# Optimization experiments

Hardware: AMD Instinct MI355X
Metric: run time of the kernel (lower is better)

The kernel has to match this reference:

```python
import jax, jax.numpy as jnp
import numpy as np

HEADS = 8
DIM_HEAD = 64
BN_EPS = 1e-5

def setup_inputs() -> dict:
    key = jax.random.key(0)
    ks = jax.random.split(key, 6)
    B, N, D = 8, 1024, 512
    inner = HEADS * DIM_HEAD  # 512
    return {
        "x": jax.random.normal(ks[0], (B, N, D), dtype=jnp.float32),
        "w_qkv": jax.random.normal(ks[1], (D, 3 * inner), dtype=jnp.float32) * (D ** -0.5),
        "conv_w": jax.random.normal(ks[2], (HEADS, HEADS), dtype=jnp.float32) * (HEADS ** -0.5),
        "conv_b": jax.random.normal(ks[3], (HEADS,), dtype=jnp.float32) * 0.02,
        "bn_gamma": jnp.ones((HEADS,), dtype=jnp.float32),
        "bn_beta": jnp.zeros((HEADS,), dtype=jnp.float32),
        "w_out": jax.random.normal(ks[4], (inner, D), dtype=jnp.float32) * (inner ** -0.5),
        "b_out": jnp.zeros((D,), dtype=jnp.float32),
    }

def reference(x, w_qkv, conv_w, conv_b, bn_gamma, bn_beta, w_out, b_out):
    B, N, D = x.shape
    H, dh = HEADS, DIM_HEAD
    scale = dh ** -0.5
    qkv = x @ w_qkv  # [B, N, 3*H*dh]
    q, k, v = jnp.split(qkv, 3, axis=-1)
    # b n (h d) -> b h n d
    q = q.reshape(B, N, H, dh).transpose(0, 2, 1, 3)
    k = k.reshape(B, N, H, dh).transpose(0, 2, 1, 3)
    v = v.reshape(B, N, H, dh).transpose(0, 2, 1, 3)
    attn = jnp.einsum('bhnd,bhmd->bhnm', q, k) * scale
    attn = jax.nn.softmax(attn, axis=-1)
    # 1x1 conv across heads (channels = heads)
    attn = jnp.einsum('gh,bhnm->bgnm', conv_w, attn) + conv_b[None, :, None, None]
    # BatchNorm2d in training mode: batch stats over (B, N, N) per head, biased variance
    mean = attn.mean(axis=(0, 2, 3), keepdims=True)
    var = attn.var(axis=(0, 2, 3), keepdims=True)
    attn = (attn - mean) * jax.lax.rsqrt(var + BN_EPS)
    attn = attn * bn_gamma[None, :, None, None] + bn_beta[None, :, None, None]
    # reatten_scale = 1.0 (transform_scale=False)
    out = jnp.einsum('bhnm,bhmd->bhnd', attn, v)
    out = out.transpose(0, 2, 1, 3).reshape(B, N, H * dh)  # b h n d -> b n (h d)
    return out @ w_out + b_out
```

## Files before the change

### kernel.cpp

```cpp
#include <hip/hip_runtime.h>
#include <math.h>


#define Bz 8
#define Nn 1024
#define Dd 512
#define Hh 8
#define DH 64
#define INNER 512
#define QW 1536
#define SCALE 0.125f
#define BN_EPS 1e-5f

typedef _Float16 __f16;
typedef __f16 f16x8 __attribute__((ext_vector_type(8)));
typedef float f32x4 __attribute__((ext_vector_type(4)));

#define MFMA16(a, b, c) __builtin_amdgcn_mfma_f32_16x16x32_f16((a), (b), (c), 0, 0, 0)

__device__ __forceinline__ unsigned short f2h(float f) {
  union { __f16 h; unsigned short s; } v;
  v.h = (__f16)f;
  return v.s;
}
__device__ __forceinline__ float h2f(unsigned short s) {
  union { unsigned short s; __f16 h; } v;
  v.s = s;
  return (float)v.h;
}

#define WB_XB 0u
#define WB_QKV 8388608u
#define WB_O1 0u
#define WB_VT 33554432u
#define WB_SG 41943040u
#define WB_O1BF WB_SG
#define WB_WQT 176160768u
#define WB_WOT 177733632u
#define WB_RSUM 178257920u
#define WB_VSUM 178520064u
#define WB_STATS 178536448u
#define WB_AC 178536512u

__global__ __launch_bounds__(256) void k_xbf(const float* __restrict__ X,
                                             unsigned short* __restrict__ XB) {
  const size_t i = ((size_t)blockIdx.x * 256 + threadIdx.x) * 8;
  float4 f0 = *(const float4*)(X + i);
  float4 f1 = *(const float4*)(X + i + 4);
  unsigned short o[8] = {f2h(f0.x), f2h(f0.y), f2h(f0.z), f2h(f0.w),
                         f2h(f1.x), f2h(f1.y), f2h(f1.z), f2h(f1.w)};
  *(uint4*)(XB + i) = *(uint4*)o;
}

__global__ __launch_bounds__(256) void k_transpose(const float* __restrict__ src,
                                                   unsigned short* __restrict__ dst,
                                                   int R, int C) {
  __shared__ float tile[32][33];
  const int tc = blockIdx.x * 32, tr = blockIdx.y * 32;
  const int lx = threadIdx.x & 31, ly = threadIdx.x >> 5;
#pragma unroll
  for (int i = 0; i < 32; i += 8)
    tile[ly + i][lx] = src[(size_t)(tr + ly + i) * C + tc + lx];
  __syncthreads();
#pragma unroll
  for (int i = 0; i < 32; i += 8)
    dst[(size_t)(tc + ly + i) * R + tr + lx] = f2h(tile[lx][ly + i]);
}

__global__ __launch_bounds__(256) void k_qkv(const unsigned short* __restrict__ XB,
                                             const unsigned short* __restrict__ WQT,
                                             unsigned short* __restrict__ qkv,
                                             unsigned short* __restrict__ vT) {
  extern __shared__ char smem[];
  unsigned short(*sA)[40] = (unsigned short(*)[40])smem;
  unsigned short(*sB)[40] = (unsigned short(*)[40])(smem + 128 * 40 * 2);
  unsigned short* sEp = (unsigned short*)smem;
  const int t = threadIdx.x;
  const int col0 = blockIdx.x * 128;
  const int row0 = blockIdx.y * 128;
  const bool isqk = (col0 < 2 * INNER);
  const int l = t & 63, w = t >> 6;
  const int wm = (w & 1) * 64, wn = (w >> 1) * 64;
  const int lm = l & 15, lq = l >> 4;
  const int srow = t >> 1, skc = (t & 1) * 16;
  f32x4 acc[4][4] = {};
  for (int k0 = 0; k0 < Dd; k0 += 32) {
    {
      const unsigned short* src = XB + (size_t)(row0 + srow) * Dd + k0 + skc;
      *(uint4*)&sA[srow][skc] = *(const uint4*)src;
      *(uint4*)&sA[srow][skc + 8] = *(const uint4*)(src + 8);
    }
    {
      const unsigned short* srcB = WQT + (size_t)(col0 + srow) * Dd + k0 + skc;
      *(uint4*)&sB[srow][skc] = *(const uint4*)srcB;
      *(uint4*)&sB[srow][skc + 8] = *(const uint4*)(srcB + 8);
    }
    __syncthreads();
    f16x8 af[4], bfr[4];
#pragma unroll
    for (int i = 0; i < 4; i++) af[i] = *(const f16x8*)&sA[wm + 16 * i + lm][lq * 8];
#pragma unroll
    for (int j = 0; j < 4; j++) bfr[j] = *(const f16x8*)&sB[wn + 16 * j + lm][lq * 8];
    if (isqk) {
#pragma unroll
      for (int i = 0; i < 4; i++)
#pragma unroll
        for (int j = 0; j < 4; j++) acc[i][j] = MFMA16(bfr[i], af[j], acc[i][j]);
    } else {
#pragma unroll
      for (int i = 0; i < 4; i++)
#pragma unroll
        for (int j = 0; j < 4; j++) acc[i][j] = MFMA16(af[i], bfr[j], acc[i][j]);
    }
    __syncthreads();
  }
  if (isqk) {
#pragma unroll
    for (int jc = 0; jc < 4; jc++)
#pragma unroll
      for (int ir = 0; ir < 4; ir++) {
        unsigned short us[4];
#pragma unroll
        for (int r = 0; r < 4; r++) us[r] = f2h(acc[jc][ir][r]);
        *(uint2*)&sEp[(wm + 16 * ir + lm) * 136 + wn + 16 * jc + 4 * lq] = *(uint2*)us;
      }
    __syncthreads();
    const int row = t >> 1, half = t & 1;
    const unsigned short* src = &sEp[row * 136 + half * 64];
    unsigned short* dst = qkv + (size_t)(row0 + row) * QW + col0 + half * 64;
#pragma unroll
    for (int c = 0; c < 8; c++) *(uint4*)(dst + c * 8) = *(const uint4*)(src + c * 8);
  } else {
#pragma unroll
    for (int ir = 0; ir < 4; ir++)
#pragma unroll
      for (int jc = 0; jc < 4; jc++) {
        unsigned short us[4];
#pragma unroll
        for (int r = 0; r < 4; r++) us[r] = f2h(acc[ir][jc][r]);
        *(uint2*)&sEp[(wn + 16 * jc + lm) * 136 + wm + 16 * ir + 4 * lq] = *(uint2*)us;
      }
    __syncthreads();
    const int row = t >> 1, half = t & 1;
    const int gd = col0 - 2 * INNER + row;
    const int bq = row0 >> 10, mseq0 = row0 & 1023;
    const unsigned short* src = &sEp[row * 136 + half * 64];
    unsigned short* dst =
        vT + (((size_t)(bq * Hh + (gd >> 6)) * DH + (gd & 63)) << 10) + mseq0 + half * 64;
#pragma unroll
    for (int c = 0; c < 8; c++) *(uint4*)(dst + c * 8) = *(const uint4*)(src + c * 8);
  }
}

__global__ __launch_bounds__(256) void k_vsum(const unsigned short* __restrict__ vT,
                                              float* __restrict__ vsum) {
  const int bg = blockIdx.x;
  const int d = threadIdx.x >> 2, qq = threadIdx.x & 3;
  __shared__ float red[64][4];
  const unsigned short* p = vT + ((size_t)bg * DH + d) * Nn + qq * 256;
  float s = 0.f;
  for (int m = 0; m < 256; m += 4) {
    uint2 rr = *(const uint2*)(p + m);
    s += h2f((unsigned short)(rr.x & 0xffff)) + h2f((unsigned short)(rr.x >> 16)) +
         h2f((unsigned short)(rr.y & 0xffff)) + h2f((unsigned short)(rr.y >> 16));
  }
  red[d][qq] = s;
  __syncthreads();
  if (threadIdx.x < 64)
    vsum[(size_t)bg * DH + threadIdx.x] =
        red[threadIdx.x][0] + red[threadIdx.x][1] + red[threadIdx.x][2] + red[threadIdx.x][3];
}

__global__ __launch_bounds__(512, 2) void k_sgen(const unsigned short* __restrict__ qkv,
                                                 unsigned short* __restrict__ Sg,
                                                 float* __restrict__ rsum) {
  __shared__ unsigned short sK[8 * 32 * 72];
  __shared__ unsigned short sT[32 * 264];
  const int b = blockIdx.x;
  const int n0 = blockIdx.y * 32;
  const int mh = blockIdx.z;
  const int t = threadIdx.x;
  const int w = t >> 6, l = t & 63;
  const int lm = l & 15, lq = l >> 4;
  f16x8 qf[2][2];
#pragma unroll
  for (int i = 0; i < 2; i++) {
    const unsigned short* qp =
        qkv + (size_t)(b * Nn + n0 + 16 * i + lm) * QW + w * DH + lq * 8;
    qf[i][0] = *(const f16x8*)qp;
    qf[i][1] = *(const f16x8*)(qp + 32);
  }
  float psum[2] = {0.f, 0.f};
  for (int it = 0; it < 16; it++) {
    const int m0 = mh * 512 + it * 32;
    {
#pragma unroll
      for (int s = 0; s < 4; s++) {
        const int c = t + s * 512;
        const int hh = c >> 8, mm = (c >> 3) & 31, qq = c & 7;
        *(uint4*)&sK[(hh * 32 + mm) * 72 + qq * 8] = *(const uint4*)(
            qkv + (size_t)(b * Nn + m0 + mm) * QW + INNER + hh * DH + qq * 8);
      }
    }
    __syncthreads();
    f32x4 lac[2][2] = {};
#pragma unroll
    for (int jm = 0; jm < 2; jm++) {
      f16x8 ka0 = *(const f16x8*)&sK[(w * 32 + 16 * jm + lm) * 72 + lq * 8];
      f16x8 ka1 = *(const f16x8*)&sK[(w * 32 + 16 * jm + lm) * 72 + 32 + lq * 8];
#pragma unroll
      for (int i = 0; i < 2; i++) {
        lac[i][jm] = MFMA16(ka0, qf[i][0], lac[i][jm]);
        lac[i][jm] = MFMA16(ka1, qf[i][1], lac[i][jm]);
      }
    }
#pragma unroll
    for (int i = 0; i < 2; i++)
#pragma unroll
      for (int jm = 0; jm < 2; jm++)
#pragma unroll
        for (int r = 0; r < 4; r++) {
          float e = __expf(lac[i][jm][r] * SCALE);
          psum[i] += e;
          sT[(16 * i + lm) * 264 + (16 * jm + 4 * lq + r) * 8 + w] = f2h(e);
        }
    __syncthreads();
    {
      const int row = t >> 4, ck = t & 15;
      unsigned short* dst =
          Sg + (((size_t)(b * Nn + n0 + row) << 10) + m0) * 8 + ck * 16;
      const unsigned short* src = &sT[row * 264 + ck * 16];
      *(uint4*)dst = *(const uint4*)src;
      *(uint4*)(dst + 8) = *(const uint4*)(src + 8);
    }
  }
#pragma unroll
  for (int i = 0; i < 2; i++) {
    psum[i] += __shfl_xor(psum[i], 16);
    psum[i] += __shfl_xor(psum[i], 32);
  }
  if (lq == 0) {
    atomicAdd(&rsum[(size_t)(b * Hh + w) * Nn + n0 + lm], psum[0]);
    atomicAdd(&rsum[(size_t)(b * Hh + w) * Nn + n0 + 16 + lm], psum[1]);
  }
}

__global__ __launch_bounds__(512, 2) void k_mixsv(const unsigned short* __restrict__ Sg,
                                                  const unsigned short* __restrict__ vT,
                                                  const float* __restrict__ rsum,
                                                  const float* __restrict__ conv_w,
                                                  float* __restrict__ O1,
                                                  float* __restrict__ stats) {
  __shared__ unsigned short sU[8][16][68];
  __shared__ float sRed[8][16];
  const int b = blockIdx.x;
  const int n0 = blockIdx.y * 16;
  const int t = threadIdx.x;
  const int w = t >> 6, l = t & 63;
  const int lm = l & 15, lq = l >> 4;
  const int mxn = t >> 5, mxm = (t & 31) * 2;
  float cw[64];
#pragma unroll
  for (int i = 0; i < 64; i++) cw[i] = conv_w[i];
  float rv[8];
#pragma unroll
  for (int h = 0; h < 8; h++) rv[h] = 1.0f / rsum[(size_t)(b * Hh + h) * Nn + n0 + mxn];
  const unsigned short* sNp = Sg + ((size_t)(b * Nn + n0 + mxn) << 13);
  f32x4 oacc[4] = {};
  float su[8] = {}, su2[8] = {};
  uint4 c0, c1;
  {
    const unsigned short* p = sNp + (mxm << 3);
    c0 = *(const uint4*)p;
    c1 = *(const uint4*)(p + 8);
  }
  for (int it = 0; it < 16; it++) {
    uint4 nx0, nx1;
    if (it < 15) {
      const unsigned short* p = sNp + ((size_t)((it + 1) * 64 + mxm) << 3);
      nx0 = *(const uint4*)p;
      nx1 = *(const uint4*)(p + 8);
    }
    {
      const unsigned* pe = (const unsigned*)&c0;
      const unsigned* po = (const unsigned*)&c1;
      float sx[8], sy[8];
#pragma unroll
      for (int hp = 0; hp < 4; hp++) {
        sx[2 * hp] = h2f((unsigned short)(pe[hp] & 0xffff)) * rv[2 * hp];
        sx[2 * hp + 1] = h2f((unsigned short)(pe[hp] >> 16)) * rv[2 * hp + 1];
        sy[2 * hp] = h2f((unsigned short)(po[hp] & 0xffff)) * rv[2 * hp];
        sy[2 * hp + 1] = h2f((unsigned short)(po[hp] >> 16)) * rv[2 * hp + 1];
      }
#pragma unroll
      for (int g = 0; g < 8; g++) {
        float u0 = 0.f, u1 = 0.f;
#pragma unroll
        for (int h = 0; h < 8; h++) {
          u0 += cw[g * 8 + h] * sx[h];
          u1 += cw[g * 8 + h] * sy[h];
        }
        su[g] += u0 + u1;
        su2[g] += u0 * u0 + u1 * u1;
        *(unsigned*)&sU[g][mxn][mxm] = (unsigned)f2h(u0) | ((unsigned)f2h(u1) << 16);
      }
    }
    __syncthreads();
    {
      f16x8 uf0 = *(const f16x8*)&sU[w][lm][lq * 8];
      f16x8 uf1 = *(const f16x8*)&sU[w][lm][32 + lq * 8];
#pragma unroll
      for (int j = 0; j < 4; j++) {
        const unsigned short* vp =
            vT + (((size_t)(b * Hh + w) * DH + 16 * j + lm) << 10) + it * 64 + lq * 8;
        f16x8 v0 = *(const f16x8*)vp;
        f16x8 v1 = *(const f16x8*)(vp + 32);
        oacc[j] = MFMA16(uf0, v0, oacc[j]);
        oacc[j] = MFMA16(uf1, v1, oacc[j]);
      }
    }
    __syncthreads();
    if (it < 15) {
      c0 = nx0;
      c1 = nx1;
    }
  }
#pragma unroll
  for (int j = 0; j < 4; j++)
#pragma unroll
    for (int r = 0; r < 4; r++)
      O1[((size_t)(b * Hh + w) * Nn + n0 + lq * 4 + r) * DH + 16 * j + lm] = oacc[j][r];
#pragma unroll
  for (int g = 0; g < 8; g++) {
    float a = su[g], q = su2[g];
    for (int off = 32; off; off >>= 1) {
      a += __shfl_down(a, off);
      q += __shfl_down(q, off);
    }
    if (l == 0) {
      sRed[w][g] = a;
      sRed[w][8 + g] = q;
    }
  }
  __syncthreads();
  if (t < 16) {
    float s = 0.f;
#pragma unroll
    for (int ww = 0; ww < 8; ww++) s += sRed[ww][t];
    atomicAdd(&stats[t], s);
  }
}

__global__ void k_alpha(const float* __restrict__ stats, const float* __restrict__ bn_gamma,
                        const float* __restrict__ bn_beta, float* __restrict__ ac) {
  const int g = threadIdx.x;
  if (g < 8) {
    const float cnt = (float)Bz * (float)Nn * (float)Nn;
    float Eu = stats[g] / cnt;
    float Eu2 = stats[8 + g] / cnt;
    float inv = rsqrtf(Eu2 - Eu * Eu + BN_EPS);
    float alpha = bn_gamma[g] * inv;
    ac[g] = alpha;
    ac[8 + g] = bn_beta[g] - Eu * alpha;
  }
}

__global__ __launch_bounds__(256) void k_o1aff(const float* __restrict__ O1,
                                               const float* __restrict__ vsum,
                                               const float* __restrict__ ac,
                                               unsigned short* __restrict__ O1BF) {
  const size_t i4 = ((size_t)blockIdx.x * 256 + threadIdx.x) * 4;
  const int bg = (int)(i4 >> 16);
  const int g = bg & 7;
  const int d = (int)(i4 & 63);
  float4 a = *(const float4*)(O1 + i4);
  float4 v = *(const float4*)(vsum + (size_t)bg * DH + d);
  const float al = ac[g], cc = ac[8 + g];
  unsigned short o[4] = {f2h(al * a.x + cc * v.x), f2h(al * a.y + cc * v.y),
                         f2h(al * a.z + cc * v.z), f2h(al * a.w + cc * v.w)};
  *(uint2*)(O1BF + i4) = *(uint2*)o;
}

__global__ __launch_bounds__(256) void k_out(const unsigned short* __restrict__ O1BF,
                                             const unsigned short* __restrict__ WOT,
                                             const float* __restrict__ bout,
                                             float* __restrict__ out) {
  __shared__ unsigned short sA[128][40];
  __shared__ unsigned short sB[128][40];
  const int t = threadIdx.x;
  const int col0 = blockIdx.x * 128, row0 = blockIdx.y * 128;
  const int l = t & 63, w = t >> 6;
  const int wm = (w & 1) * 64, wn = (w >> 1) * 64;
  const int lm = l & 15, lq = l >> 4;
  const int srow = t >> 1, skc = (t & 1) * 16;
  const int b = row0 >> 10;
  const int nn = (row0 + srow) & 1023;
  f32x4 acc[4][4] = {};
  for (int k0 = 0; k0 < INNER; k0 += 32) {
    {
      const int k = k0 + skc;
      const int g = k >> 6, dd = k & 63;
      const unsigned short* src = O1BF + ((size_t)(b * Hh + g) * Nn + nn) * DH + dd;
      *(uint4*)&sA[srow][skc] = *(const uint4*)src;
      *(uint4*)&sA[srow][skc + 8] = *(const uint4*)(src + 8);
    }
    {
      const unsigned short* srcB = WOT + (size_t)(col0 + srow) * INNER + k0 + skc;
      *(uint4*)&sB[srow][skc] = *(const uint4*)srcB;
      *(uint4*)&sB[srow][skc + 8] = *(const uint4*)(srcB + 8);
    }
    __syncthreads();
    f16x8 af[4], bfr[4];
#pragma unroll
    for (int i = 0; i < 4; i++) af[i] = *(const f16x8*)&sA[wm + 16 * i + lm][lq * 8];
#pragma unroll
    for (int j = 0; j < 4; j++) bfr[j] = *(const f16x8*)&sB[wn + 16 * j + lm][lq * 8];
#pragma unroll
    for (int i = 0; i < 4; i++)
#pragma unroll
      for (int j = 0; j < 4; j++) acc[i][j] = MFMA16(af[i], bfr[j], acc[i][j]);
    __syncthreads();
  }
#pragma unroll
  for (int j = 0; j < 4; j++) {
    const int col = col0 + wn + 16 * j + lm;
    const float bo = bout[col];
#pragma unroll
    for (int i = 0; i < 4; i++) {
      const int rbase = row0 + wm + 16 * i + lq * 4;
#pragma unroll
      for (int r = 0; r < 4; r++) out[(size_t)(rbase + r) * Dd + col] = acc[i][j][r] + bo;
    }
  }
}

extern "C" void kernel_launch(void* const* d_in, const int* in_sizes, int n_in,
                              void* d_out, int out_size, void* d_ws, size_t ws_size,
                              hipStream_t stream) {
  const float* x = (const float*)d_in[0];
  const float* w_qkv = (const float*)d_in[1];
  const float* conv_w = (const float*)d_in[2];
  const float* bn_gamma = (const float*)d_in[4];
  const float* bn_beta = (const float*)d_in[5];
  const float* w_out = (const float*)d_in[6];
  const float* b_out = (const float*)d_in[7];
  char* ws = (char*)d_ws;
  unsigned short* XB = (unsigned short*)(ws + WB_XB);
  unsigned short* QKV = (unsigned short*)(ws + WB_QKV);
  unsigned short* VT = (unsigned short*)(ws + WB_VT);
  unsigned short* SG = (unsigned short*)(ws + WB_SG);
  unsigned short* WQT = (unsigned short*)(ws + WB_WQT);
  unsigned short* WOT = (unsigned short*)(ws + WB_WOT);
  float* O1 = (float*)(ws + WB_O1);
  unsigned short* O1BF = (unsigned short*)(ws + WB_O1BF);
  float* RSUM = (float*)(ws + WB_RSUM);
  float* VSUM = (float*)(ws + WB_VSUM);
  float* STATS = (float*)(ws + WB_STATS);
  float* AC = (float*)(ws + WB_AC);

  hipMemsetAsync(STATS, 0, 64, stream);
  hipMemsetAsync(RSUM, 0, 262144, stream);
  k_xbf<<<2048, 256, 0, stream>>>(x, XB);
  k_transpose<<<dim3(48, 16), 256, 0, stream>>>(w_qkv, WQT, 512, 1536);
  k_transpose<<<dim3(16, 16), 256, 0, stream>>>(w_out, WOT, 512, 512);
  k_qkv<<<dim3(12, 64), 256, 34816, stream>>>(XB, WQT, QKV, VT);
  k_vsum<<<64, 256, 0, stream>>>(VT, VSUM);
  k_sgen<<<dim3(8, 32, 2), 512, 0, stream>>>(QKV, SG, RSUM);
  k_mixsv<<<dim3(8, 64), 512, 0, stream>>>(SG, VT, RSUM, conv_w, O1, STATS);
  k_alpha<<<1, 64, 0, stream>>>(STATS, bn_gamma, bn_beta, AC);
  k_o1aff<<<4096, 256, 0, stream>>>(O1, VSUM, AC, O1BF);
  k_out<<<dim3(4, 64), 256, 0, stream>>>(O1BF, WOT, b_out, (float*)d_out);
}
```

Measured before the change: 271.7 us.

## Chunk batch through sgen/mixsv and split mixsv over key halves

The score-generation and mix/SV stages now process the batch in two chunks of four, so the intermediate exp-score buffer is half as large and more likely to stay in the last-level cache between the producer and consumer kernels. mixsv also gains a grid dimension that splits the key range into two halves, writing separate partial outputs that the affine kernel sums. It double-buffers the shared U tile so one barrier per iteration can be dropped. The cost is extra kernel launches, an extra fp32 partial output buffer to read, and less parallelism per launch.

After: 303.1 us. 1.12x slower.

```diff
diff --git a/kernel.cpp b/kernel.cpp
--- a/kernel.cpp
+++ b/kernel.cpp
@@ -31,16 +31,17 @@
 
 #define WB_XB 0u
 #define WB_QKV 8388608u
-#define WB_O1 0u
 #define WB_VT 33554432u
 #define WB_SG 41943040u
-#define WB_O1BF WB_SG
-#define WB_WQT 176160768u
-#define WB_WOT 177733632u
-#define WB_RSUM 178257920u
-#define WB_VSUM 178520064u
-#define WB_STATS 178536448u
-#define WB_AC 178536512u
+#define WB_O1A 109051904u
+#define WB_O1B 125829120u
+#define WB_O1BF 142606336u
+#define WB_WQT 150994944u
+#define WB_WOT 152567808u
+#define WB_RSUM 153092096u
+#define WB_VSUM 153354240u
+#define WB_STATS 153370624u
+#define WB_AC 153370688u
 
 __global__ __launch_bounds__(256) void k_xbf(const float* __restrict__ X,
                                              unsigned short* __restrict__ XB) {
@@ -173,12 +174,12 @@
 
 __global__ __launch_bounds__(512, 2) void k_sgen(const unsigned short* __restrict__ qkv,
                                                  unsigned short* __restrict__ Sg,
-                                                 float* __restrict__ rsum) {
+                                                 float* __restrict__ rsum, int b0) {
   __shared__ unsigned short sK[8 * 32 * 72];
   __shared__ unsigned short sT[32 * 264];
-  const int b = blockIdx.x;
+  const int bl = blockIdx.x, b = b0 + bl;
   const int n0 = blockIdx.y * 32;
-  const int mh = blockIdx.z;
+  const int mq = blockIdx.z;
   const int t = threadIdx.x;
   const int w = t >> 6, l = t & 63;
   const int lm = l & 15, lq = l >> 4;
@@ -191,8 +192,8 @@
     qf[i][1] = *(const f16x8*)(qp + 32);
   }
   float psum[2] = {0.f, 0.f};
-  for (int it = 0; it < 16; it++) {
-    const int m0 = mh * 512 + it * 32;
+  for (int it = 0; it < 8; it++) {
+    const int m0 = mq * 256 + it * 32;
     {
 #pragma unroll
       for (int s = 0; s < 4; s++) {
@@ -228,7 +229,7 @@
     {
       const int row = t >> 4, ck = t & 15;
       unsigned short* dst =
-          Sg + (((size_t)(b * Nn + n0 + row) << 10) + m0) * 8 + ck * 16;
+          Sg + (((size_t)(bl * Nn + n0 + row) << 10) + m0) * 8 + ck * 16;
       const unsigned short* src = &sT[row * 264 + ck * 16];
       *(uint4*)dst = *(const uint4*)src;
       *(uint4*)(dst + 8) = *(const uint4*)(src + 8);
@@ -249,12 +250,15 @@
                                                   const unsigned short* __restrict__ vT,
                                                   const float* __restrict__ rsum,
                                                   const float* __restrict__ conv_w,
-                                                  float* __restrict__ O1,
-                                                  float* __restrict__ stats) {
-  __shared__ unsigned short sU[8][16][68];
+                                                  float* __restrict__ O1A,
+                                                  float* __restrict__ O1B,
+                                                  float* __restrict__ stats, int b0) {
+  __shared__ unsigned short sU[2][8][16][68];
   __shared__ float sRed[8][16];
-  const int b = blockIdx.x;
+  const int bl = blockIdx.x, b = b0 + bl;
   const int n0 = blockIdx.y * 16;
+  const int mbase = blockIdx.z * 512;
+  float* __restrict__ O1 = blockIdx.z ? O1B : O1A;
   const int t = threadIdx.x;
   const int w = t >> 6, l = t & 63;
   const int lm = l & 15, lq = l >> 4;
@@ -265,19 +269,20 @@
   float rv[8];
 #pragma unroll
   for (int h = 0; h < 8; h++) rv[h] = 1.0f / rsum[(size_t)(b * Hh + h) * Nn + n0 + mxn];
-  const unsigned short* sNp = Sg + ((size_t)(b * Nn + n0 + mxn) << 13);
+  const unsigned short* sNp = Sg + ((size_t)(bl * Nn + n0 + mxn) << 13);
   f32x4 oacc[4] = {};
   float su[8] = {}, su2[8] = {};
   uint4 c0, c1;
   {
-    const unsigned short* p = sNp + (mxm << 3);
+    const unsigned short* p = sNp + ((size_t)(mbase + mxm) << 3);
     c0 = *(const uint4*)p;
     c1 = *(const uint4*)(p + 8);
   }
-  for (int it = 0; it < 16; it++) {
+  for (int it = 0; it < 8; it++) {
+    const int cur = it & 1;
     uint4 nx0, nx1;
-    if (it < 15) {
-      const unsigned short* p = sNp + ((size_t)((it + 1) * 64 + mxm) << 3);
+    if (it < 7) {
+      const unsigned short* p = sNp + ((size_t)(mbase + (it + 1) * 64 + mxm) << 3);
       nx0 = *(const uint4*)p;
       nx1 = *(const uint4*)(p + 8);
     }
@@ -302,25 +307,24 @@
         }
         su[g] += u0 + u1;
         su2[g] += u0 * u0 + u1 * u1;
-        *(unsigned*)&sU[g][mxn][mxm] = (unsigned)f2h(u0) | ((unsigned)f2h(u1) << 16);
-      }
-    }
-    __syncthreads();
-    {
-      f16x8 uf0 = *(const f16x8*)&sU[w][lm][lq * 8];
-      f16x8 uf1 = *(const f16x8*)&sU[w][lm][32 + lq * 8];
+        *(unsigned*)&sU[cur][g][mxn][mxm] = (unsigned)f2h(u0) | ((unsigned)f2h(u1) << 16);
+      }
+    }
+    __syncthreads();
+    {
+      f16x8 uf0 = *(const f16x8*)&sU[cur][w][lm][lq * 8];
+      f16x8 uf1 = *(const f16x8*)&sU[cur][w][lm][32 + lq * 8];
 #pragma unroll
       for (int j = 0; j < 4; j++) {
         const unsigned short* vp =
-            vT + (((size_t)(b * Hh + w) * DH + 16 * j + lm) << 10) + it * 64 + lq * 8;
+            vT + (((size_t)(b * Hh + w) * DH + 16 * j + lm) << 10) + mbase + it * 64 + lq * 8;
         f16x8 v0 = *(const f16x8*)vp;
         f16x8 v1 = *(const f16x8*)(vp + 32);
         oacc[j] = MFMA16(uf0, v0, oacc[j]);
         oacc[j] = MFMA16(uf1, v1, oacc[j]);
       }
     }
-    __syncthreads();
-    if (it < 15) {
+    if (it < 7) {
       c0 = nx0;
       c1 = nx1;
     }
@@ -365,7 +369,8 @@
   }
 }
 
-__global__ __launch_bounds__(256) void k_o1aff(const float* __restrict__ O1,
+__global__ __launch_bounds__(256) void k_o1aff(const float* __restrict__ O1A,
+                                               const float* __restrict__ O1B,
                                                const float* __restrict__ vsum,
                                                const float* __restrict__ ac,
                                                unsigned short* __restrict__ O1BF) {
@@ -373,11 +378,12 @@
   const int bg = (int)(i4 >> 16);
   const int g = bg & 7;
   const int d = (int)(i4 & 63);
-  float4 a = *(const float4*)(O1 + i4);
+  float4 a = *(const float4*)(O1A + i4);
+  float4 bb = *(const float4*)(O1B + i4);
   float4 v = *(const float4*)(vsum + (size_t)bg * DH + d);
   const float al = ac[g], cc = ac[8 + g];
-  unsigned short o[4] = {f2h(al * a.x + cc * v.x), f2h(al * a.y + cc * v.y),
-                         f2h(al * a.z + cc * v.z), f2h(al * a.w + cc * v.w)};
+  unsigned short o[4] = {f2h(al * (a.x + bb.x) + cc * v.x), f2h(al * (a.y + bb.y) + cc * v.y),
+                         f2h(al * (a.z + bb.z) + cc * v.z), f2h(al * (a.w + bb.w) + cc * v.w)};
   *(uint2*)(O1BF + i4) = *(uint2*)o;
 }
 
@@ -451,7 +457,8 @@
   unsigned short* SG = (unsigned short*)(ws + WB_SG);
   unsigned short* WQT = (unsigned short*)(ws + WB_WQT);
   unsigned short* WOT = (unsigned short*)(ws + WB_WOT);
-  float* O1 = (float*)(ws + WB_O1);
+  float* O1Ap = (float*)(ws + WB_O1A);
+  float* O1Bp = (float*)(ws + WB_O1B);
   unsigned short* O1BF = (unsigned short*)(ws + WB_O1BF);
   float* RSUM = (float*)(ws + WB_RSUM);
   float* VSUM = (float*)(ws + WB_VSUM);
@@ -465,9 +472,12 @@
   k_transpose<<<dim3(16, 16), 256, 0, stream>>>(w_out, WOT, 512, 512);
   k_qkv<<<dim3(12, 64), 256, 34816, stream>>>(XB, WQT, QKV, VT);
   k_vsum<<<64, 256, 0, stream>>>(VT, VSUM);
-  k_sgen<<<dim3(8, 32, 2), 512, 0, stream>>>(QKV, SG, RSUM);
-  k_mixsv<<<dim3(8, 64), 512, 0, stream>>>(SG, VT, RSUM, conv_w, O1, STATS);
+  for (int c = 0; c < 2; c++) {
+    k_sgen<<<dim3(4, 32, 4), 512, 0, stream>>>(QKV, SG, RSUM, c * 4);
+    k_mixsv<<<dim3(4, 64, 2), 512, 0, stream>>>(SG, VT, RSUM, conv_w, O1Ap, O1Bp,
+                                                STATS, c * 4);
+  }
   k_alpha<<<1, 64, 0, stream>>>(STATS, bn_gamma, bn_beta, AC);
-  k_o1aff<<<4096, 256, 0, stream>>>(O1, VSUM, AC, O1BF);
+  k_o1aff<<<4096, 256, 0, stream>>>(O1Ap, O1Bp, VSUM, AC, O1BF);
   k_out<<<dim3(4, 64), 256, 0, stream>>>(O1BF, WOT, b_out, (float*)d_out);
 }
```

## Recompute QK^T scores in fused mix kernel instead of materialising exp-score tensor

Applied to the files above, without the earlier changes.

Removes the large fp16 exp-score buffer (B*N*N*H) that was written by k_sgen and read back by k_mixsv. A new k_rsum pass computes the softmax row sums and their reciprocals with no atomics. k_fuse then recomputes QK^T per tile, normalises, applies the head-mixing conv, and multiplies by V in the same kernel. This trades roughly twice the QK^T MFMA work and extra K reloads from global memory for eliminating about 134MB of HBM write plus read traffic. The memset of the row-sum buffer is also removed.

Result: slower. 337.6 us (+24.3%).

```diff
diff --git a/kernel.cpp b/kernel.cpp
--- a/kernel.cpp
+++ b/kernel.cpp
@@ -31,16 +31,15 @@
 
 #define WB_XB 0u
 #define WB_QKV 8388608u
-#define WB_O1 0u
 #define WB_VT 33554432u
-#define WB_SG 41943040u
-#define WB_O1BF WB_SG
-#define WB_WQT 176160768u
-#define WB_WOT 177733632u
-#define WB_RSUM 178257920u
-#define WB_VSUM 178520064u
-#define WB_STATS 178536448u
-#define WB_AC 178536512u
+#define WB_O1 41943040u
+#define WB_O1BF 58720256u
+#define WB_WQT 67108864u
+#define WB_WOT 68681728u
+#define WB_RINV 69206016u
+#define WB_VSUM 69468160u
+#define WB_STATS 69484544u
+#define WB_AC 69484608u
 
 __global__ __launch_bounds__(256) void k_xbf(const float* __restrict__ X,
                                              unsigned short* __restrict__ XB) {
@@ -171,158 +170,116 @@
         red[threadIdx.x][0] + red[threadIdx.x][1] + red[threadIdx.x][2] + red[threadIdx.x][3];
 }
 
-__global__ __launch_bounds__(512, 2) void k_sgen(const unsigned short* __restrict__ qkv,
-                                                 unsigned short* __restrict__ Sg,
-                                                 float* __restrict__ rsum) {
-  __shared__ unsigned short sK[8 * 32 * 72];
-  __shared__ unsigned short sT[32 * 264];
+__global__ __launch_bounds__(512, 2) void k_rsum(const unsigned short* __restrict__ qkv,
+                                                 float* __restrict__ rinv) {
   const int b = blockIdx.x;
-  const int n0 = blockIdx.y * 32;
-  const int mh = blockIdx.z;
+  const int n0 = blockIdx.y * 16;
   const int t = threadIdx.x;
   const int w = t >> 6, l = t & 63;
   const int lm = l & 15, lq = l >> 4;
-  f16x8 qf[2][2];
-#pragma unroll
-  for (int i = 0; i < 2; i++) {
-    const unsigned short* qp =
-        qkv + (size_t)(b * Nn + n0 + 16 * i + lm) * QW + w * DH + lq * 8;
-    qf[i][0] = *(const f16x8*)qp;
-    qf[i][1] = *(const f16x8*)(qp + 32);
-  }
-  float psum[2] = {0.f, 0.f};
-  for (int it = 0; it < 16; it++) {
-    const int m0 = mh * 512 + it * 32;
-    {
-#pragma unroll
-      for (int s = 0; s < 4; s++) {
-        const int c = t + s * 512;
-        const int hh = c >> 8, mm = (c >> 3) & 31, qq = c & 7;
-        *(uint4*)&sK[(hh * 32 + mm) * 72 + qq * 8] = *(const uint4*)(
-            qkv + (size_t)(b * Nn + m0 + mm) * QW + INNER + hh * DH + qq * 8);
-      }
-    }
-    __syncthreads();
-    f32x4 lac[2][2] = {};
+  f16x8 qf[2];
+  {
+    const unsigned short* qp = qkv + (size_t)(b * Nn + n0 + lm) * QW + w * DH + lq * 8;
+    qf[0] = *(const f16x8*)qp;
+    qf[1] = *(const f16x8*)(qp + 32);
+  }
+  float psum[4] = {};
+  for (int m0 = 0; m0 < Nn; m0 += 32) {
 #pragma unroll
     for (int jm = 0; jm < 2; jm++) {
-      f16x8 ka0 = *(const f16x8*)&sK[(w * 32 + 16 * jm + lm) * 72 + lq * 8];
-      f16x8 ka1 = *(const f16x8*)&sK[(w * 32 + 16 * jm + lm) * 72 + 32 + lq * 8];
-#pragma unroll
-      for (int i = 0; i < 2; i++) {
-        lac[i][jm] = MFMA16(ka0, qf[i][0], lac[i][jm]);
-        lac[i][jm] = MFMA16(ka1, qf[i][1], lac[i][jm]);
-      }
-    }
-#pragma unroll
-    for (int i = 0; i < 2; i++)
-#pragma unroll
-      for (int jm = 0; jm < 2; jm++)
-#pragma unroll
-        for (int r = 0; r < 4; r++) {
-          float e = __expf(lac[i][jm][r] * SCALE);
-          psum[i] += e;
-          sT[(16 * i + lm) * 264 + (16 * jm + 4 * lq + r) * 8 + w] = f2h(e);
-        }
-    __syncthreads();
-    {
-      const int row = t >> 4, ck = t & 15;
-      unsigned short* dst =
-          Sg + (((size_t)(b * Nn + n0 + row) << 10) + m0) * 8 + ck * 16;
-      const unsigned short* src = &sT[row * 264 + ck * 16];
-      *(uint4*)dst = *(const uint4*)src;
-      *(uint4*)(dst + 8) = *(const uint4*)(src + 8);
-    }
-  }
-#pragma unroll
-  for (int i = 0; i < 2; i++) {
-    psum[i] += __shfl_xor(psum[i], 16);
-    psum[i] += __shfl_xor(psum[i], 32);
-  }
-  if (lq == 0) {
-    atomicAdd(&rsum[(size_t)(b * Hh + w) * Nn + n0 + lm], psum[0]);
-    atomicAdd(&rsum[(size_t)(b * Hh + w) * Nn + n0 + 16 + lm], psum[1]);
-  }
-}
-
-__global__ __launch_bounds__(512, 2) void k_mixsv(const unsigned short* __restrict__ Sg,
-                                                  const unsigned short* __restrict__ vT,
-                                                  const float* __restrict__ rsum,
-                                                  const float* __restrict__ conv_w,
-                                                  float* __restrict__ O1,
-                                                  float* __restrict__ stats) {
-  __shared__ unsigned short sU[8][16][68];
+      const unsigned short* kp =
+          qkv + (size_t)(b * Nn + m0 + 16 * jm + lm) * QW + INNER + w * DH + lq * 8;
+      f16x8 k0 = *(const f16x8*)kp;
+      f16x8 k1 = *(const f16x8*)(kp + 32);
+      f32x4 lac = {};
+      lac = MFMA16(qf[0], k0, lac);
+      lac = MFMA16(qf[1], k1, lac);
+#pragma unroll
+      for (int r = 0; r < 4; r++) psum[r] += __expf(lac[r] * SCALE);
+    }
+  }
+#pragma unroll
+  for (int r = 0; r < 4; r++) {
+    float s = psum[r];
+    s += __shfl_xor(s, 1);
+    s += __shfl_xor(s, 2);
+    s += __shfl_xor(s, 4);
+    s += __shfl_xor(s, 8);
+    if (lm == 0) rinv[(size_t)(b * Hh + w) * Nn + n0 + lq * 4 + r] = 1.0f / s;
+  }
+}
+
+__global__ __launch_bounds__(512, 2) void k_fuse(const unsigned short* __restrict__ qkv,
+                                                 const unsigned short* __restrict__ vT,
+                                                 const float* __restrict__ rinv,
+                                                 const float* __restrict__ conv_w,
+                                                 float* __restrict__ O1,
+                                                 float* __restrict__ stats) {
+  __shared__ __align__(16) unsigned short sS[8][16][36];
+  __shared__ __align__(16) unsigned short sU[8][16][40];
   __shared__ float sRed[8][16];
   const int b = blockIdx.x;
   const int n0 = blockIdx.y * 16;
   const int t = threadIdx.x;
   const int w = t >> 6, l = t & 63;
   const int lm = l & 15, lq = l >> 4;
-  const int mxn = t >> 5, mxm = (t & 31) * 2;
+  const int mxn = t >> 5, mxm = t & 31;
   float cw[64];
 #pragma unroll
   for (int i = 0; i < 64; i++) cw[i] = conv_w[i];
-  float rv[8];
-#pragma unroll
-  for (int h = 0; h < 8; h++) rv[h] = 1.0f / rsum[(size_t)(b * Hh + h) * Nn + n0 + mxn];
-  const unsigned short* sNp = Sg + ((size_t)(b * Nn + n0 + mxn) << 13);
+  f16x8 qf[2];
+  {
+    const unsigned short* qp = qkv + (size_t)(b * Nn + n0 + lm) * QW + w * DH + lq * 8;
+    qf[0] = *(const f16x8*)qp;
+    qf[1] = *(const f16x8*)(qp + 32);
+  }
+  float rv[4];
+#pragma unroll
+  for (int r = 0; r < 4; r++)
+    rv[r] = rinv[(size_t)(b * Hh + w) * Nn + n0 + lq * 4 + r];
   f32x4 oacc[4] = {};
   float su[8] = {}, su2[8] = {};
-  uint4 c0, c1;
-  {
-    const unsigned short* p = sNp + (mxm << 3);
-    c0 = *(const uint4*)p;
-    c1 = *(const uint4*)(p + 8);
-  }
-  for (int it = 0; it < 16; it++) {
-    uint4 nx0, nx1;
-    if (it < 15) {
-      const unsigned short* p = sNp + ((size_t)((it + 1) * 64 + mxm) << 3);
-      nx0 = *(const uint4*)p;
-      nx1 = *(const uint4*)(p + 8);
-    }
-    {
-      const unsigned* pe = (const unsigned*)&c0;
-      const unsigned* po = (const unsigned*)&c1;
-      float sx[8], sy[8];
-#pragma unroll
-      for (int hp = 0; hp < 4; hp++) {
-        sx[2 * hp] = h2f((unsigned short)(pe[hp] & 0xffff)) * rv[2 * hp];
-        sx[2 * hp + 1] = h2f((unsigned short)(pe[hp] >> 16)) * rv[2 * hp + 1];
-        sy[2 * hp] = h2f((unsigned short)(po[hp] & 0xffff)) * rv[2 * hp];
-        sy[2 * hp + 1] = h2f((unsigned short)(po[hp] >> 16)) * rv[2 * hp + 1];
+  for (int m0 = 0; m0 < Nn; m0 += 32) {
+    {
+#pragma unroll
+      for (int jm = 0; jm < 2; jm++) {
+        const unsigned short* kp =
+            qkv + (size_t)(b * Nn + m0 + 16 * jm + lm) * QW + INNER + w * DH + lq * 8;
+        f16x8 k0 = *(const f16x8*)kp;
+        f16x8 k1 = *(const f16x8*)(kp + 32);
+        f32x4 lac = {};
+        lac = MFMA16(qf[0], k0, lac);
+        lac = MFMA16(qf[1], k1, lac);
+#pragma unroll
+        for (int r = 0; r < 4; r++)
+          sS[w][lq * 4 + r][16 * jm + lm] = f2h(__expf(lac[r] * SCALE) * rv[r]);
       }
+    }
+    __syncthreads();
+    {
+      float sv[8];
+#pragma unroll
+      for (int h = 0; h < 8; h++) sv[h] = h2f(sS[h][mxn][mxm]);
 #pragma unroll
       for (int g = 0; g < 8; g++) {
-        float u0 = 0.f, u1 = 0.f;
-#pragma unroll
-        for (int h = 0; h < 8; h++) {
-          u0 += cw[g * 8 + h] * sx[h];
-          u1 += cw[g * 8 + h] * sy[h];
-        }
-        su[g] += u0 + u1;
-        su2[g] += u0 * u0 + u1 * u1;
-        *(unsigned*)&sU[g][mxn][mxm] = (unsigned)f2h(u0) | ((unsigned)f2h(u1) << 16);
+        float u = 0.f;
+#pragma unroll
+        for (int h = 0; h < 8; h++) u += cw[g * 8 + h] * sv[h];
+        su[g] += u;
+        su2[g] += u * u;
+        sU[g][mxn][mxm] = f2h(u);
       }
     }
     __syncthreads();
     {
-      f16x8 uf0 = *(const f16x8*)&sU[w][lm][lq * 8];
-      f16x8 uf1 = *(const f16x8*)&sU[w][lm][32 + lq * 8];
+      f16x8 uf = *(const f16x8*)&sU[w][lm][lq * 8];
 #pragma unroll
       for (int j = 0; j < 4; j++) {
         const unsigned short* vp =
-            vT + (((size_t)(b * Hh + w) * DH + 16 * j + lm) << 10) + it * 64 + lq * 8;
-        f16x8 v0 = *(const f16x8*)vp;
-        f16x8 v1 = *(const f16x8*)(vp + 32);
-        oacc[j] = MFMA16(uf0, v0, oacc[j]);
-        oacc[j] = MFMA16(uf1, v1, oacc[j]);
+            vT + (((size_t)(b * Hh + w) * DH + 16 * j + lm) << 10) + m0 + lq * 8;
+        f16x8 vv = *(const f16x8*)vp;
+        oacc[j] = MFMA16(uf, vv, oacc[j]);
       }
-    }
-    __syncthreads();
-    if (it < 15) {
-      c0 = nx0;
-      c1 = nx1;
     }
   }
 #pragma unroll
@@ -448,25 +405,23 @@
   unsigned short* XB = (unsigned short*)(ws + WB_XB);
   unsigned short* QKV = (unsigned short*)(ws + WB_QKV);
   unsigned short* VT = (unsigned short*)(ws + WB_VT);
-  unsigned short* SG = (unsigned short*)(ws + WB_SG);
   unsigned short* WQT = (unsigned short*)(ws + WB_WQT);
   unsigned short* WOT = (unsigned short*)(ws + WB_WOT);
   float* O1 = (float*)(ws + WB_O1);
   unsigned short* O1BF = (unsigned short*)(ws + WB_O1BF);
-  float* RSUM = (float*)(ws + WB_RSUM);
+  float* RINV = (float*)(ws + WB_RINV);
   float* VSUM = (float*)(ws + WB_VSUM);
   float* STATS = (float*)(ws + WB_STATS);
   float* AC = (float*)(ws + WB_AC);
 
   hipMemsetAsync(STATS, 0, 64, stream);
-  hipMemsetAsync(RSUM, 0, 262144, stream);
   k_xbf<<<2048, 256, 0, stream>>>(x, XB);
   k_transpose<<<dim3(48, 16), 256, 0, stream>>>(w_qkv, WQT, 512, 1536);
   k_transpose<<<dim3(16, 16), 256, 0, stream>>>(w_out, WOT, 512, 512);
   k_qkv<<<dim3(12, 64), 256, 34816, stream>>>(XB, WQT, QKV, VT);
   k_vsum<<<64, 256, 0, stream>>>(VT, VSUM);
-  k_sgen<<<dim3(8, 32, 2), 512, 0, stream>>>(QKV, SG, RSUM);
-  k_mixsv<<<dim3(8, 64), 512, 0, stream>>>(SG, VT, RSUM, conv_w, O1, STATS);
+  k_rsum<<<dim3(8, 64), 512, 0, stream>>>(QKV, RINV);
+  k_fuse<<<dim3(8, 64), 512, 0, stream>>>(QKV, VT, RINV, conv_w, O1, STATS);
   k_alpha<<<1, 64, 0, stream>>>(STATS, bn_gamma, bn_beta, AC);
   k_o1aff<<<4096, 256, 0, stream>>>(O1, VSUM, AC, O1BF);
   k_out<<<dim3(4, 64), 256, 0, stream>>>(O1BF, WOT, b_out, (float*)d_out);
```
